# Optimization experiments

Hardware: AMD Instinct MI355X
Metric: run time of the kernel (lower is better)

## Reference

```python
import jax, jax.numpy as jnp
import numpy as np

N_NODES = 100000
N_EDGES = 1600000
IN_DIM = 4
HID = 64


def gcn_conv(x, src, dst, W, b, num_nodes):
    """PyG GCNConv: out = D^-1/2 (A+I) D^-1/2 (x @ W) + b, add aggregation."""
    loop = jnp.arange(num_nodes)
    src_f = jnp.concatenate([src, loop])  # [E+N]
    dst_f = jnp.concatenate([dst, loop])
    # degree from destination (col) counts, self loops included -> deg >= 1
    deg = jax.ops.segment_sum(jnp.ones_like(dst_f, dtype=x.dtype), dst_f,
                              num_segments=num_nodes)
    dinv = jax.lax.rsqrt(deg)
    norm = dinv[src_f] * dinv[dst_f]  # [E+N]
    h = x @ W  # [N, out] transform first (cheaper when out <= in is false too; matches PyG)
    msg = h[src_f] * norm[:, None]  # [E+N, out]
    out = jax.ops.segment_sum(msg, dst_f, num_segments=num_nodes)
    return out + b


def setup_inputs() -> dict:
    key = jax.random.key(0)
    ks = jax.random.split(key, 6)
    x = jax.random.normal(ks[0], (N_NODES, IN_DIM), dtype=jnp.float32)
    edge_index = jax.random.randint(ks[1], (2, N_EDGES), 0, N_NODES, dtype=jnp.int64)
    # glorot-ish scaled weights
    W1 = jax.random.normal(ks[2], (IN_DIM, HID), dtype=jnp.float32) / np.sqrt(IN_DIM)
    b1 = jnp.zeros((HID,), dtype=jnp.float32)
    W2 = jax.random.normal(ks[3], (HID, HID), dtype=jnp.float32) / np.sqrt(HID)
    b2 = jnp.zeros((HID,), dtype=jnp.float32)
    Wl = jax.random.normal(ks[4], (HID, 1), dtype=jnp.float32) / np.sqrt(HID)
    bl = jnp.zeros((1,), dtype=jnp.float32)
    return {"x": x, "edge_index": edge_index, "W1": W1, "b1": b1,
            "W2": W2, "b2": b2, "Wl": Wl, "bl": bl}


def reference(x, edge_index, W1, b1, W2, b2, Wl, bl):
    num_nodes = x.shape[0]
    src, dst = edge_index[0], edge_index[1]
    h = jax.nn.relu(gcn_conv(x, src, dst, W1, b1, num_nodes))
    h = jax.nn.relu(gcn_conv(h, src, dst, W2, b2, num_nodes))
    logits = (h @ Wl + bl).squeeze(-1)  # [N]
    return logits
```

## Files before the change

### kernel.cpp

```cpp
#include <hip/hip_runtime.h>

#define NN 100000
#define NE 1600000
#define HID 64
#define NBUK 391
#define SRCBITS 17
#define SRCMASK 0x1FFFF
#define EBLK 2048
#define GE2 ((NE + EBLK - 1) / EBLK)
#define SCANN (NBUK * GE2)
#define CHUNK 1024
#define NCH ((SCANN + CHUNK - 1) / CHUNK)

typedef __attribute__((ext_vector_type(8))) short bf16x8;
typedef __attribute__((ext_vector_type(4))) float f32x4;

__device__ __forceinline__ float bf2f(unsigned short u) {
    return __uint_as_float(((unsigned int)u) << 16);
}
__device__ __forceinline__ unsigned short f2bf(float f) {
    unsigned int x = __float_as_uint(f);
    return (unsigned short)((x + 0x7FFFu + ((x >> 16) & 1u)) >> 16);
}
__device__ __forceinline__ float bflo(unsigned int u) { return __uint_as_float(u << 16); }
__device__ __forceinline__ float bfhi(unsigned int u) { return __uint_as_float(u & 0xFFFF0000u); }

__device__ __forceinline__ int ld_idx(const int* __restrict__ ei, int off, int is64) {
    return is64 ? ei[2 * off] : ei[off];
}

__device__ __forceinline__ int detect_flag(const int* __restrict__ ei, int t, int* sflag) {
    if (t < 64) {
        unsigned long long b = __ballot(ei[2 * t + 1] != 0);
        if (t == 0) *sflag = (b == 0ULL) ? 1 : 0;
    }
    __syncthreads();
    return *sflag;
}

__global__ void k_histA(const int* __restrict__ ei, int* __restrict__ histG) {
    __shared__ int hist[NBUK];
    __shared__ int sflag;
    int t = threadIdx.x;
    for (int i = t; i < NBUK; i += 256) hist[i] = 0;
    int f = detect_flag(ei, t, &sflag);
    int base = blockIdx.x * EBLK;
#pragma unroll
    for (int k = 0; k < EBLK / 256; ++k) {
        int e = base + k * 256 + t;
        if (e < NE) {
            int d = ld_idx(ei, NE + e, f);
            atomicAdd(&hist[d >> 8], 1);
        }
    }
    __syncthreads();
    for (int i = t; i < NBUK; i += 256) histG[i * GE2 + blockIdx.x] = hist[i];
}

__global__ void k_scan1(int* __restrict__ g, int* __restrict__ bsum) {
    __shared__ int s[256];
    int t = threadIdx.x;
    int i4 = blockIdx.x * 256 + t;
    int base = i4 * 4;
    int4 v = make_int4(0, 0, 0, 0);
    if (base + 3 < SCANN) v = ((const int4*)g)[i4];
    else {
        if (base + 0 < SCANN) v.x = g[base + 0];
        if (base + 1 < SCANN) v.y = g[base + 1];
        if (base + 2 < SCANN) v.z = g[base + 2];
        if (base + 3 < SCANN) v.w = g[base + 3];
    }
    int tsum = v.x + v.y + v.z + v.w;
    s[t] = tsum; __syncthreads();
    for (int off = 1; off < 256; off <<= 1) {
        int u = (t >= off) ? s[t - off] : 0;
        __syncthreads();
        s[t] += u;
        __syncthreads();
    }
    int run = s[t] - tsum;
    int4 o;
    o.x = run; run += v.x;
    o.y = run; run += v.y;
    o.z = run; run += v.z;
    o.w = run;
    if (base + 3 < SCANN) ((int4*)g)[i4] = o;
    else {
        if (base + 0 < SCANN) g[base + 0] = o.x;
        if (base + 1 < SCANN) g[base + 1] = o.y;
        if (base + 2 < SCANN) g[base + 2] = o.z;
        if (base + 3 < SCANN) g[base + 3] = o.w;
    }
    if (t == 255) bsum[blockIdx.x] = s[255];
}

__global__ void k_scan2(int* __restrict__ bsum) {
    __shared__ int s[512];
    int t = threadIdx.x;
    int v = (t < NCH) ? bsum[t] : 0;
    s[t] = v; __syncthreads();
    for (int off = 1; off < 512; off <<= 1) {
        int u = (t >= off) ? s[t - off] : 0;
        __syncthreads();
        s[t] += u;
        __syncthreads();
    }
    if (t < NCH) bsum[t] = s[t] - v;
}

__global__ void k_fillA(const int* __restrict__ ei, const int* __restrict__ histS,
                        const int* __restrict__ bsum, unsigned int* __restrict__ bbuf) {
    __shared__ int cur[NBUK];
    __shared__ int sflag;
    int t = threadIdx.x;
    for (int i = t; i < NBUK; i += 256) {
        int idx = i * GE2 + blockIdx.x;
        cur[i] = histS[idx] + bsum[idx >> 10];
    }
    int f = detect_flag(ei, t, &sflag);
    int base = blockIdx.x * EBLK;
#pragma unroll
    for (int k = 0; k < EBLK / 256; ++k) {
        int e = base + k * 256 + t;
        if (e < NE) {
            int s = ld_idx(ei, e, f);
            int d = ld_idx(ei, NE + e, f);
            int p = atomicAdd(&cur[d >> 8], 1);
            bbuf[p] = ((unsigned int)(d & 255) << SRCBITS) | (unsigned int)s;
        }
    }
}

__global__ void k_passB(const unsigned int* __restrict__ bbuf, const int* __restrict__ histS,
                        const int* __restrict__ bsum, const float* __restrict__ x,
                        int* __restrict__ cnt, int* __restrict__ offs,
                        float* __restrict__ dinv, float* __restrict__ xs,
                        int* __restrict__ csr) {
    __shared__ int hist[256];
    __shared__ int scn[256];
    __shared__ int cur[256];
    int t = threadIdx.x;
    int b = blockIdx.x;
    int i0 = b * GE2;
    int base = histS[i0] + bsum[i0 >> 10];
    int next = (b == NBUK - 1) ? NE : (histS[i0 + GE2] + bsum[(i0 + GE2) >> 10]);
    int sz = next - base;
    const unsigned int* buf = bbuf + base;
    hist[t] = 0;
    __syncthreads();
    for (int e = t; e < sz; e += 256)
        atomicAdd(&hist[buf[e] >> SRCBITS], 1);
    __syncthreads();
    int deg = hist[t];
    scn[t] = deg; __syncthreads();
    for (int off = 1; off < 256; off <<= 1) {
        int u = (t >= off) ? scn[t - off] : 0;
        __syncthreads();
        scn[t] += u;
        __syncthreads();
    }
    int myoff = base + scn[t] - deg;
    int node = b * 256 + t;
    if (node < NN) {
        cnt[node]  = deg;
        offs[node] = myoff;
        float d = 1.0f / sqrtf((float)(deg + 1));
        dinv[node] = d;
        float4 xv = ((const float4*)x)[node];
        float4 o; o.x = d * xv.x; o.y = d * xv.y; o.z = d * xv.z; o.w = d * xv.w;
        ((float4*)xs)[node] = o;
    }
    cur[t] = myoff;
    __syncthreads();
    for (int e = t; e < sz; e += 256) {
        unsigned int u = buf[e];
        int p = atomicAdd(&cur[u >> SRCBITS], 1);
        csr[p] = (int)(u & SRCMASK);
    }
}

__global__ void k_mm2(const float* __restrict__ xs, const int* __restrict__ cnt,
                      const int* __restrict__ offs, const int* __restrict__ csr,
                      const float* __restrict__ dinv,
                      const float* __restrict__ W1, const float* __restrict__ b1,
                      const float* __restrict__ W2, unsigned short* __restrict__ hs) {
    __shared__ unsigned short h1b[64 * 72];
    __shared__ unsigned short w2t[64 * 72];
    __shared__ float4 sPart[256];
    __shared__ float4 sAgg[64];
    __shared__ float4 sXs[64];
    __shared__ float sW1[256];
    __shared__ float sb1[64];
    __shared__ float sdv[64];
    __shared__ int scnt[64];
    __shared__ int soff[64];
    int t = threadIdx.x;
    int base = blockIdx.x * 64;
    if (t < 64) {
        int g = base + t;
        bool ok = (g < NN);
        scnt[t] = ok ? cnt[g] : 0;
        soff[t] = ok ? offs[g] : 0;
        sdv[t]  = ok ? dinv[g] : 0.f;
        sXs[t]  = ok ? ((const float4*)xs)[g] : make_float4(0.f, 0.f, 0.f, 0.f);
        sb1[t]  = b1[t];
    }
    sW1[t] = W1[t];
    for (int i = t; i < 4096; i += 256) {
        int k = i >> 6, n = i & 63;
        w2t[n * 72 + k] = f2bf(W2[i]);
    }
    if (blockIdx.x == 0 && t >= 128 && t < 192) hs[NN * 64 + (t - 128)] = 0;
    __syncthreads();
    {
        int node_l = t & 63, part = t >> 6;
        int n = scnt[node_l], b0 = soff[node_l];
        float4 s = make_float4(0.f, 0.f, 0.f, 0.f);
        int j = part;
        for (; j + 8 <= n; j += 8) {
            int s0 = csr[b0 + j], s1 = csr[b0 + j + 4];
            float4 v0 = ((const float4*)xs)[s0];
            float4 v1 = ((const float4*)xs)[s1];
            s.x += v0.x + v1.x; s.y += v0.y + v1.y;
            s.z += v0.z + v1.z; s.w += v0.w + v1.w;
        }
        for (; j < n; j += 4) {
            int s0 = csr[b0 + j];
            float4 v = ((const float4*)xs)[s0];
            s.x += v.x; s.y += v.y; s.z += v.z; s.w += v.w;
        }
        sPart[t] = s;
    }
    __syncthreads();
    if (t < 64) {
        float4 a = sPart[t], b = sPart[t + 64], c = sPart[t + 128], d = sPart[t + 192];
        float4 xi = sXs[t];
        float dn = sdv[t];
        float4 o;
        o.x = dn * (a.x + b.x + c.x + d.x + xi.x);
        o.y = dn * (a.y + b.y + c.y + d.y + xi.y);
        o.z = dn * (a.z + b.z + c.z + d.z + xi.z);
        o.w = dn * (a.w + b.w + c.w + d.w + xi.w);
        sAgg[t] = o;
    }
    __syncthreads();
#pragma unroll
    for (int i = 0; i < 16; ++i) {
        int e = i * 256 + t;
        int nl = e >> 6, c = e & 63;
        float4 a = sAgg[nl];
        float h = fmaf(a.x, sW1[c], fmaf(a.y, sW1[64 + c],
                  fmaf(a.z, sW1[128 + c], fmaf(a.w, sW1[192 + c], sb1[c]))));
        h1b[nl * 72 + c] = f2bf(fmaxf(h, 0.f));
    }
    __syncthreads();
    int w = t >> 6, lane = t & 63, l15 = lane & 15, quad = lane >> 4;
    bf16x8 a0 = *(const bf16x8*)&h1b[(w * 16 + l15) * 72 + quad * 8];
    bf16x8 a1 = *(const bf16x8*)&h1b[(w * 16 + l15) * 72 + 32 + quad * 8];
    f32x4 acc[4];
#pragma unroll
    for (int nt = 0; nt < 4; ++nt) {
        bf16x8 bb0 = *(const bf16x8*)&w2t[(nt * 16 + l15) * 72 + quad * 8];
        bf16x8 bb1 = *(const bf16x8*)&w2t[(nt * 16 + l15) * 72 + 32 + quad * 8];
        f32x4 c = {0.f, 0.f, 0.f, 0.f};
        c = __builtin_amdgcn_mfma_f32_16x16x32_bf16(a0, bb0, c, 0, 0, 0);
        c = __builtin_amdgcn_mfma_f32_16x16x32_bf16(a1, bb1, c, 0, 0, 0);
        acc[nt] = c;
    }
#pragma unroll
    for (int nt = 0; nt < 4; ++nt) {
#pragma unroll
        for (int r = 0; r < 4; ++r) {
            int localn = w * 16 + quad * 4 + r;
            int g = base + localn;
            if (g < NN) hs[g * 64 + nt * 16 + l15] = f2bf(acc[nt][r] * sdv[localn]);
        }
    }
}

__global__ void k_gather_head(const unsigned short* __restrict__ hs, const int* __restrict__ offs,
                              const int* __restrict__ cnt, const int* __restrict__ csr,
                              const float* __restrict__ dinv, const float* __restrict__ b2,
                              const float* __restrict__ Wl, const float* __restrict__ bl,
                              float* __restrict__ out) {
    int t = threadIdx.x;
    int node = blockIdx.x * 4 + (t >> 6);
    int c = t & 63;
    int qg = c >> 4;
    int ql = c & 15;
    int b = offs[node], n = cnt[node];
    const uint2* hrow = (const uint2*)hs;
    int myidx = (c < n) ? csr[b + c] : NN;
    int m = n < 64 ? n : 64;
    float4 A = make_float4(0.f, 0.f, 0.f, 0.f);
    float4 B = make_float4(0.f, 0.f, 0.f, 0.f);
    for (int j = 0; j < m; j += 16) {
        int s0 = __shfl(myidx, j + qg, 64);
        int s1 = __shfl(myidx, j + 4 + qg, 64);
        int s2 = __shfl(myidx, j + 8 + qg, 64);
        int s3 = __shfl(myidx, j + 12 + qg, 64);
        uint2 u0 = hrow[s0 * 16 + ql];
        uint2 u1 = hrow[s1 * 16 + ql];
        uint2 u2 = hrow[s2 * 16 + ql];
        uint2 u3 = hrow[s3 * 16 + ql];
        A.x += bflo(u0.x); A.y += bfhi(u0.x); A.z += bflo(u0.y); A.w += bfhi(u0.y);
        B.x += bflo(u1.x); B.y += bfhi(u1.x); B.z += bflo(u1.y); B.w += bfhi(u1.y);
        A.x += bflo(u2.x); A.y += bfhi(u2.x); A.z += bflo(u2.y); A.w += bfhi(u2.y);
        B.x += bflo(u3.x); B.y += bfhi(u3.x); B.z += bflo(u3.y); B.w += bfhi(u3.y);
    }
    for (int j = 64; j < n; j += 4) {
        int e = j + qg;
        int s = (e < n) ? csr[b + e] : NN;
        uint2 u = hrow[s * 16 + ql];
        A.x += bflo(u.x); A.y += bfhi(u.x); A.z += bflo(u.y); A.w += bfhi(u.y);
    }
    float4 S;
    S.x = A.x + B.x; S.y = A.y + B.y; S.z = A.z + B.z; S.w = A.w + B.w;
    S.x += __shfl_xor(S.x, 16, 64); S.x += __shfl_xor(S.x, 32, 64);
    S.y += __shfl_xor(S.y, 16, 64); S.y += __shfl_xor(S.y, 32, 64);
    S.z += __shfl_xor(S.z, 16, 64); S.z += __shfl_xor(S.z, 32, 64);
    S.w += __shfl_xor(S.w, 16, 64); S.w += __shfl_xor(S.w, 32, 64);
    uint2 uS = hrow[node * 16 + ql];
    S.x += bflo(uS.x); S.y += bfhi(uS.x); S.z += bflo(uS.y); S.w += bfhi(uS.y);
    float4 bv = ((const float4*)b2)[ql];
    float4 wv = ((const float4*)Wl)[ql];
    float dn = dinv[node];
    float v = fmaxf(fmaf(dn, S.x, bv.x), 0.f) * wv.x
            + fmaxf(fmaf(dn, S.y, bv.y), 0.f) * wv.y
            + fmaxf(fmaf(dn, S.z, bv.z), 0.f) * wv.z
            + fmaxf(fmaf(dn, S.w, bv.w), 0.f) * wv.w;
#pragma unroll
    for (int off = 8; off; off >>= 1) v += __shfl_down(v, off, 16);
    if (c == 0) out[node] = v + bl[0];
}

extern "C" void kernel_launch(void* const* d_in, const int* in_sizes, int n_in,
                              void* d_out, int out_size, void* d_ws, size_t ws_size,
                              hipStream_t stream) {
    const float* x  = (const float*)d_in[0];
    const int*   ei = (const int*)d_in[1];
    const float* W1 = (const float*)d_in[2];
    const float* b1 = (const float*)d_in[3];
    const float* W2 = (const float*)d_in[4];
    const float* b2 = (const float*)d_in[5];
    const float* Wl = (const float*)d_in[6];
    const float* bl = (const float*)d_in[7];
    float* out = (float*)d_out;

    char* w = (char*)d_ws;
    float* dinv  = (float*)w;                  w += NN * 4;
    int*   cnt   = (int*)w;                    w += NN * 4;
    int*   offs  = (int*)w;                    w += NN * 4;
    int*   csr   = (int*)w;                    w += NE * 4;
    float* xs    = (float*)w;                  w += NN * 4 * 4;
    unsigned short* hs = (unsigned short*)w;   w += (size_t)(NN + 1) * HID * 2;
    int*   histG = (int*)w;                    w += (size_t)((SCANN + 3) & ~3) * 4;
    int*   bsum  = (int*)w;                    w += 512 * 4;
    unsigned int* bbuf = (unsigned int*)w;     w += (size_t)NE * 4;

    const int GMM = (NN + 63) / 64;

    hipLaunchKernelGGL(k_histA,  dim3(GE2),  dim3(256), 0, stream, ei, histG);
    hipLaunchKernelGGL(k_scan1,  dim3(NCH),  dim3(256), 0, stream, histG, bsum);
    hipLaunchKernelGGL(k_scan2,  dim3(1),    dim3(512), 0, stream, bsum);
    hipLaunchKernelGGL(k_fillA,  dim3(GE2),  dim3(256), 0, stream, ei, histG, bsum, bbuf);
    hipLaunchKernelGGL(k_passB,  dim3(NBUK), dim3(256), 0, stream,
                       bbuf, histG, bsum, x, cnt, offs, dinv, xs, csr);
    hipLaunchKernelGGL(k_mm2, dim3(GMM), dim3(256), 0, stream,
                       xs, cnt, offs, csr, dinv, W1, b1, W2, hs);
    hipLaunchKernelGGL(k_gather_head, dim3(NN / 4), dim3(256), 0, stream,
                       hs, offs, cnt, csr, dinv, b2, Wl, bl, out);
}
```

Measured before the change: 180.2 us.

## Fuse layer-1 feature aggregation into CSR scatter pass using LDS float atomics

The old bucket pass is split in two. The first computes degrees, offsets, dinv and the scaled features. The second scatters CSR entries and also accumulates the layer-1 4-wide neighbour sums into shared-memory float atomics per destination bucket, then writes an aggregated feature array. The matmul kernel then reads that precomputed aggregate instead of walking the CSR again. This removes a separate irregular CSR gather pass, but adds one kernel launch, an extra pass over bbuf, many LDS float atomics, and nondeterministic summation order.

```diff
diff --git a/kernel.cpp b/kernel.cpp
--- a/kernel.cpp
+++ b/kernel.cpp
@@ -131,14 +131,12 @@
     }
 }
 
-__global__ void k_passB(const unsigned int* __restrict__ bbuf, const int* __restrict__ histS,
-                        const int* __restrict__ bsum, const float* __restrict__ x,
-                        int* __restrict__ cnt, int* __restrict__ offs,
-                        float* __restrict__ dinv, float* __restrict__ xs,
-                        int* __restrict__ csr) {
+__global__ void k_passB1(const unsigned int* __restrict__ bbuf, const int* __restrict__ histS,
+                         const int* __restrict__ bsum, const float* __restrict__ x,
+                         int* __restrict__ cnt, int* __restrict__ offs,
+                         float* __restrict__ dinv, float* __restrict__ xs) {
     __shared__ int hist[256];
     __shared__ int scn[256];
-    __shared__ int cur[256];
     int t = threadIdx.x;
     int b = blockIdx.x;
     int i0 = b * GE2;
@@ -159,51 +157,95 @@
         scn[t] += u;
         __syncthreads();
     }
-    int myoff = base + scn[t] - deg;
     int node = b * 256 + t;
     if (node < NN) {
         cnt[node]  = deg;
-        offs[node] = myoff;
+        offs[node] = base + scn[t] - deg;
         float d = 1.0f / sqrtf((float)(deg + 1));
         dinv[node] = d;
         float4 xv = ((const float4*)x)[node];
         float4 o; o.x = d * xv.x; o.y = d * xv.y; o.z = d * xv.z; o.w = d * xv.w;
         ((float4*)xs)[node] = o;
     }
-    cur[t] = myoff;
-    __syncthreads();
-    for (int e = t; e < sz; e += 256) {
-        unsigned int u = buf[e];
-        int p = atomicAdd(&cur[u >> SRCBITS], 1);
-        csr[p] = (int)(u & SRCMASK);
-    }
-}
-
-__global__ void k_mm2(const float* __restrict__ xs, const int* __restrict__ cnt,
-                      const int* __restrict__ offs, const int* __restrict__ csr,
-                      const float* __restrict__ dinv,
-                      const float* __restrict__ W1, const float* __restrict__ b1,
-                      const float* __restrict__ W2, unsigned short* __restrict__ hs) {
+}
+
+__global__ void k_passB2(const unsigned int* __restrict__ bbuf, const int* __restrict__ histS,
+                         const int* __restrict__ bsum, const float* __restrict__ xs,
+                         const int* __restrict__ offs, const float* __restrict__ dinv,
+                         int* __restrict__ csr, float* __restrict__ agg) {
+    __shared__ int cur[256];
+    __shared__ float sacc[1024];
+    int t = threadIdx.x;
+    int b = blockIdx.x;
+    int i0 = b * GE2;
+    int base = histS[i0] + bsum[i0 >> 10];
+    int next = (b == NBUK - 1) ? NE : (histS[i0 + GE2] + bsum[(i0 + GE2) >> 10]);
+    int node = b * 256 + t;
+    cur[t] = (node < NN) ? offs[node] : 0;
+    sacc[t] = 0.f; sacc[t + 256] = 0.f; sacc[t + 512] = 0.f; sacc[t + 768] = 0.f;
+    __syncthreads();
+    int e = base + t;
+    for (; e + 768 < next; e += 1024) {
+        unsigned int u0 = bbuf[e];
+        unsigned int u1 = bbuf[e + 256];
+        unsigned int u2 = bbuf[e + 512];
+        unsigned int u3 = bbuf[e + 768];
+        int s0 = u0 & SRCMASK, s1 = u1 & SRCMASK, s2 = u2 & SRCMASK, s3 = u3 & SRCMASK;
+        float4 v0 = ((const float4*)xs)[s0];
+        float4 v1 = ((const float4*)xs)[s1];
+        float4 v2 = ((const float4*)xs)[s2];
+        float4 v3 = ((const float4*)xs)[s3];
+        int d0 = u0 >> SRCBITS, d1 = u1 >> SRCBITS, d2 = u2 >> SRCBITS, d3 = u3 >> SRCBITS;
+        int p0 = atomicAdd(&cur[d0], 1); csr[p0] = s0;
+        int p1 = atomicAdd(&cur[d1], 1); csr[p1] = s1;
+        int p2 = atomicAdd(&cur[d2], 1); csr[p2] = s2;
+        int p3 = atomicAdd(&cur[d3], 1); csr[p3] = s3;
+        atomicAdd(&sacc[d0], v0.x); atomicAdd(&sacc[d0 + 256], v0.y);
+        atomicAdd(&sacc[d0 + 512], v0.z); atomicAdd(&sacc[d0 + 768], v0.w);
+        atomicAdd(&sacc[d1], v1.x); atomicAdd(&sacc[d1 + 256], v1.y);
+        atomicAdd(&sacc[d1 + 512], v1.z); atomicAdd(&sacc[d1 + 768], v1.w);
+        atomicAdd(&sacc[d2], v2.x); atomicAdd(&sacc[d2 + 256], v2.y);
+        atomicAdd(&sacc[d2 + 512], v2.z); atomicAdd(&sacc[d2 + 768], v2.w);
+        atomicAdd(&sacc[d3], v3.x); atomicAdd(&sacc[d3 + 256], v3.y);
+        atomicAdd(&sacc[d3 + 512], v3.z); atomicAdd(&sacc[d3 + 768], v3.w);
+    }
+    for (; e < next; e += 256) {
+        unsigned int u = bbuf[e];
+        int s = u & SRCMASK, d = u >> SRCBITS;
+        float4 v = ((const float4*)xs)[s];
+        int p = atomicAdd(&cur[d], 1); csr[p] = s;
+        atomicAdd(&sacc[d], v.x); atomicAdd(&sacc[d + 256], v.y);
+        atomicAdd(&sacc[d + 512], v.z); atomicAdd(&sacc[d + 768], v.w);
+    }
+    __syncthreads();
+    if (node < NN) {
+        float4 xi = ((const float4*)xs)[node];
+        float dn = dinv[node];
+        float4 o;
+        o.x = dn * (sacc[t]       + xi.x);
+        o.y = dn * (sacc[t + 256] + xi.y);
+        o.z = dn * (sacc[t + 512] + xi.z);
+        o.w = dn * (sacc[t + 768] + xi.w);
+        ((float4*)agg)[node] = o;
+    }
+}
+
+__global__ void k_mm(const float* __restrict__ agg, const float* __restrict__ W1,
+                     const float* __restrict__ b1, const float* __restrict__ W2,
+                     const float* __restrict__ dinv, unsigned short* __restrict__ hs) {
     __shared__ unsigned short h1b[64 * 72];
     __shared__ unsigned short w2t[64 * 72];
-    __shared__ float4 sPart[256];
     __shared__ float4 sAgg[64];
-    __shared__ float4 sXs[64];
     __shared__ float sW1[256];
     __shared__ float sb1[64];
-    __shared__ float sdv[64];
-    __shared__ int scnt[64];
-    __shared__ int soff[64];
+    __shared__ float sDinv[64];
     int t = threadIdx.x;
     int base = blockIdx.x * 64;
     if (t < 64) {
         int g = base + t;
-        bool ok = (g < NN);
-        scnt[t] = ok ? cnt[g] : 0;
-        soff[t] = ok ? offs[g] : 0;
-        sdv[t]  = ok ? dinv[g] : 0.f;
-        sXs[t]  = ok ? ((const float4*)xs)[g] : make_float4(0.f, 0.f, 0.f, 0.f);
-        sb1[t]  = b1[t];
+        sAgg[t]  = (g < NN) ? ((const float4*)agg)[g] : make_float4(0.f, 0.f, 0.f, 0.f);
+        sDinv[t] = (g < NN) ? dinv[g] : 0.f;
+        sb1[t]   = b1[t];
     }
     sW1[t] = W1[t];
     for (int i = t; i < 4096; i += 256) {
@@ -212,41 +254,9 @@
     }
     if (blockIdx.x == 0 && t >= 128 && t < 192) hs[NN * 64 + (t - 128)] = 0;
     __syncthreads();
-    {
-        int node_l = t & 63, part = t >> 6;
-        int n = scnt[node_l], b0 = soff[node_l];
-        float4 s = make_float4(0.f, 0.f, 0.f, 0.f);
-        int j = part;
-        for (; j + 8 <= n; j += 8) {
-            int s0 = csr[b0 + j], s1 = csr[b0 + j + 4];
-            float4 v0 = ((const float4*)xs)[s0];
-            float4 v1 = ((const float4*)xs)[s1];
-            s.x += v0.x + v1.x; s.y += v0.y + v1.y;
-            s.z += v0.z + v1.z; s.w += v0.w + v1.w;
-        }
-        for (; j < n; j += 4) {
-            int s0 = csr[b0 + j];
-            float4 v = ((const float4*)xs)[s0];
-            s.x += v.x; s.y += v.y; s.z += v.z; s.w += v.w;
-        }
-        sPart[t] = s;
-    }
-    __syncthreads();
-    if (t < 64) {
-        float4 a = sPart[t], b = sPart[t + 64], c = sPart[t + 128], d = sPart[t + 192];
-        float4 xi = sXs[t];
-        float dn = sdv[t];
-        float4 o;
-        o.x = dn * (a.x + b.x + c.x + d.x + xi.x);
-        o.y = dn * (a.y + b.y + c.y + d.y + xi.y);
-        o.z = dn * (a.z + b.z + c.z + d.z + xi.z);
-        o.w = dn * (a.w + b.w + c.w + d.w + xi.w);
-        sAgg[t] = o;
-    }
-    __syncthreads();
 #pragma unroll
     for (int i = 0; i < 16; ++i) {
-        int e = i * 256 + t;
+        int e = t + i * 256;
         int nl = e >> 6, c = e & 63;
         float4 a = sAgg[nl];
         float h = fmaf(a.x, sW1[c], fmaf(a.y, sW1[64 + c],
@@ -273,7 +283,7 @@
         for (int r = 0; r < 4; ++r) {
             int localn = w * 16 + quad * 4 + r;
             int g = base + localn;
-            if (g < NN) hs[g * 64 + nt * 16 + l15] = f2bf(acc[nt][r] * sdv[localn]);
+            if (g < NN) hs[g * 64 + nt * 16 + l15] = f2bf(acc[nt][r] * sDinv[localn]);
         }
     }
 }
@@ -353,6 +363,7 @@
     int*   offs  = (int*)w;                    w += NN * 4;
     int*   csr   = (int*)w;                    w += NE * 4;
     float* xs    = (float*)w;                  w += NN * 4 * 4;
+    float* agg   = (float*)w;                  w += NN * 4 * 4;
     unsigned short* hs = (unsigned short*)w;   w += (size_t)(NN + 1) * HID * 2;
     int*   histG = (int*)w;                    w += (size_t)((SCANN + 3) & ~3) * 4;
     int*   bsum  = (int*)w;                    w += 512 * 4;
@@ -364,10 +375,12 @@
     hipLaunchKernelGGL(k_scan1,  dim3(NCH),  dim3(256), 0, stream, histG, bsum);
     hipLaunchKernelGGL(k_scan2,  dim3(1),    dim3(512), 0, stream, bsum);
     hipLaunchKernelGGL(k_fillA,  dim3(GE2),  dim3(256), 0, stream, ei, histG, bsum, bbuf);
-    hipLaunchKernelGGL(k_passB,  dim3(NBUK), dim3(256), 0, stream,
-                       bbuf, histG, bsum, x, cnt, offs, dinv, xs, csr);
-    hipLaunchKernelGGL(k_mm2, dim3(GMM), dim3(256), 0, stream,
-                       xs, cnt, offs, csr, dinv, W1, b1, W2, hs);
+    hipLaunchKernelGGL(k_passB1, dim3(NBUK), dim3(256), 0, stream,
+                       bbuf, histG, bsum, x, cnt, offs, dinv, xs);
+    hipLaunchKernelGGL(k_passB2, dim3(NBUK), dim3(256), 0, stream,
+                       bbuf, histG, bsum, xs, offs, dinv, csr, agg);
+    hipLaunchKernelGGL(k_mm, dim3(GMM), dim3(256), 0, stream,
+                       agg, W1, b1, W2, dinv, hs);
     hipLaunchKernelGGL(k_gather_head, dim3(NN / 4), dim3(256), 0, stream,
                        hs, offs, cnt, csr, dinv, b2, Wl, bl, out);
 }
```

After: 208.7 us. 1.16x slower.
